# Performance work log

Hardware: AMD Instinct MI355X
Metric: run time of the kernel (lower is better)

The kernel has to match this reference:

```python
import jax, jax.numpy as jnp
import numpy as np

NUM_AUTHORS = 100000
NUM_PAPERS = 150000
EMB_DIM = 64
N_EDGES = 3200000
BATCH = 65536
EPS = 1e-8


def setup_inputs() -> dict:
    key = jax.random.key(0)
    k = jax.random.split(key, 6)
    return {
        "author_emb": jax.random.normal(k[0], (NUM_AUTHORS, EMB_DIM), dtype=jnp.float32) * 0.01,
        "paper_emb": jax.random.normal(k[1], (NUM_PAPERS, EMB_DIM), dtype=jnp.float32) * 0.01,
        "authors": jax.random.randint(k[2], (BATCH,), 0, NUM_AUTHORS),
        "papers": jax.random.randint(k[3], (BATCH,), 0, NUM_PAPERS),
        "edge_author": jax.random.randint(k[4], (N_EDGES,), 0, NUM_AUTHORS),
        "edge_paper": jax.random.randint(k[5], (N_EDGES,), 0, NUM_PAPERS),
    }


def _write_conv(a_emb, p_emb, edge_author, edge_paper, norm, u_sw, i_sw):
    """GCN-style bipartite conv with symmetric degree normalization and
    degree-gated self term (u_sw/i_sw ~= 1 only for isolated nodes)."""
    # messages author -> paper over 'like' edges
    msg_ap = a_emb[edge_author] * norm[:, None]            # [E, D]
    new_p = i_sw * p_emb + jax.ops.segment_sum(msg_ap, edge_paper, num_segments=NUM_PAPERS)
    # messages paper -> author over 'rev_like' edges
    msg_pa = p_emb[edge_paper] * norm[:, None]             # [E, D]
    new_a = u_sw * a_emb + jax.ops.segment_sum(msg_pa, edge_author, num_segments=NUM_AUTHORS)
    return new_a, new_p


def reference(author_emb, paper_emb, authors, papers, edge_author, edge_paper):
    ones_e = jnp.ones((N_EDGES,), dtype=jnp.float32)
    author_deg = jax.ops.segment_sum(ones_e, edge_author, num_segments=NUM_AUTHORS)  # out-deg 'like'
    paper_deg = jax.ops.segment_sum(ones_e, edge_paper, num_segments=NUM_PAPERS)     # out-deg 'rev_like'
    u_sw = (1.0 - author_deg / (author_deg + EPS))[:, None]   # [Na, 1]
    i_sw = (1.0 - paper_deg / (paper_deg + EPS))[:, None]     # [Np, 1]
    # symmetric normalization per edge: 1/sqrt(deg_a * deg_p)
    norm = jax.lax.rsqrt((author_deg[edge_author] + EPS) * (paper_deg[edge_paper] + EPS))  # [E]

    a1, p1 = _write_conv(author_emb, paper_emb, edge_author, edge_paper, norm, u_sw, i_sw)
    a2, p2 = _write_conv(a1, p1, edge_author, edge_paper, norm, u_sw, i_sw)

    final_author = author_emb + a1 + a2   # l_author = [0,1,2]
    final_paper = paper_emb + p1 + p2     # l_paper = [0,1,2]

    latest_author = final_author[authors]  # [B, D]
    latest_paper = final_paper[papers]     # [B, D]
    predict = jax.nn.sigmoid(jnp.sum(latest_author * latest_paper, axis=1))  # [B]
    return predict, latest_author, latest_paper
```

## Files before the change

kernel.cpp:

```cpp
#include <hip/hip_runtime.h>
#include <hip/hip_bf16.h>
#include <math.h>

#define NA 100000
#define NP 150000
#define EMB 64
#define NE 3200000
#define BATCH 65536
#define EPS 1e-8f
#define F8 128.0f
#define INVF8 (1.0f / 128.0f)

#define SH_A 8
#define SH_P 9
#define NB_A ((NA + (1 << SH_A) - 1) >> SH_A)
#define NB_P ((NP + (1 << SH_P) - 1) >> SH_P)
#define NBT (NB_A + NB_P)
#define CAP_A 9216
#define CAP_P 12288
#define TOT_A (NB_A * CAP_A)
#define TOT_P (NB_P * CAP_P)
#define PACK_SH 18
#define PACK_MASK ((1u << PACK_SH) - 1)
#define CHUNK 8192

typedef float f32x2 __attribute__((ext_vector_type(2)));

#if defined(__has_builtin)
#if __has_builtin(__builtin_amdgcn_cvt_pk_f32_fp8) && __has_builtin(__builtin_amdgcn_cvt_pk_fp8_f32)
#define HW_FP8 1
#endif
#endif

__device__ inline unsigned pk_fp8x4(float a, float b, float c, float d) {
#ifdef HW_FP8
    int t = __builtin_amdgcn_cvt_pk_fp8_f32(a, b, 0, false);
    t = __builtin_amdgcn_cvt_pk_fp8_f32(c, d, t, true);
    return (unsigned)t;
#else
    auto enc = [](float x) -> unsigned {
        union { float f; unsigned u; } t; t.f = x;
        unsigned s = t.u >> 31; int e = (int)((t.u >> 23) & 0xFF) - 127;
        unsigned m = (t.u >> 20) & 7;
        int E = e + 7;
        if (E <= 0) return s << 7;
        if (E > 15) { E = 15; m = 7; }
        return (s << 7) | ((unsigned)E << 3) | m;
    };
    return enc(a) | (enc(b) << 8) | (enc(c) << 16) | (enc(d) << 24);
#endif
}

__device__ inline f32x2 up_fp8x2(unsigned v, bool hi) {
#ifdef HW_FP8
    return hi ? __builtin_amdgcn_cvt_pk_f32_fp8((int)v, true)
              : __builtin_amdgcn_cvt_pk_f32_fp8((int)v, false);
#else
    auto dec = [](unsigned b) -> float {
        unsigned s = b >> 7, e = (b >> 3) & 0xF, m = b & 7;
        if (e == 0) return (s ? -1.0f : 1.0f) * (float)m * 0.001953125f;
        union { unsigned u; float f; } t;
        t.u = (s << 31) | ((e + 120) << 23) | (m << 20);
        return t.f;
    };
    unsigned sh = hi ? 16 : 0;
    f32x2 r;
    r.x = dec((v >> sh) & 0xFF);
    r.y = dec((v >> (sh + 8)) & 0xFF);
    return r;
#endif
}

__device__ inline unsigned pack_bf16(float a, float b) {
    __hip_bfloat16 ha = __float2bfloat16(a);
    __hip_bfloat16 hb = __float2bfloat16(b);
    unsigned ua = *(unsigned short*)&ha;
    unsigned ub = *(unsigned short*)&hb;
    return ua | (ub << 16);
}

__device__ inline float bf_lo(unsigned u) { return __uint_as_float(u << 16); }
__device__ inline float bf_hi(unsigned u) { return __uint_as_float(u & 0xffff0000u); }


__global__ void init_cur(int* __restrict__ bcur, uint2* __restrict__ sa0,
                         uint2* __restrict__ sp0, uint2* __restrict__ sa1,
                         uint2* __restrict__ sp1) {
    int i = blockIdx.x * blockDim.x + threadIdx.x;
    if (i < NB_A) bcur[i] = i * CAP_A;
    else if (i < NBT) bcur[i] = (i - NB_A) * CAP_P;
    if (i < 8)       sa0[(size_t)NA * 8 + i]        = uint2{0, 0};
    else if (i < 16) sp0[(size_t)NP * 8 + (i - 8)]  = uint2{0, 0};
    else if (i < 24) sa1[(size_t)NA * 8 + (i - 16)] = uint2{0, 0};
    else if (i < 32) sp1[(size_t)NP * 8 + (i - 24)] = uint2{0, 0};
}


__global__ void stage_kernel(const int* __restrict__ ea, const int* __restrict__ ep,
                             int* __restrict__ bcur,
                             unsigned* __restrict__ stg_a, unsigned* __restrict__ stg_p) {
    __shared__ int h[NBT];
    __shared__ int lcur[NBT];
    int t = threadIdx.x;
    for (int i = t; i < NBT; i += blockDim.x) h[i] = 0;
    __syncthreads();
    int e0 = blockIdx.x * CHUNK;
    int e1 = min(e0 + CHUNK, NE);
    for (int e = e0 + t; e < e1; e += blockDim.x) {
        atomicAdd(&h[ea[e] >> SH_A], 1);
        atomicAdd(&h[NB_A + (ep[e] >> SH_P)], 1);
    }
    __syncthreads();
    for (int i = t; i < NBT; i += blockDim.x) {
        int c = h[i];
        h[i] = c ? atomicAdd(&bcur[i], c) : 0;
        lcur[i] = 0;
    }
    __syncthreads();
    for (int e = e0 + t; e < e1; e += blockDim.x) {
        int a = ea[e], p = ep[e];
        int ba = a >> SH_A;
        int bp = NB_A + (p >> SH_P);
        int la = atomicAdd(&lcur[ba], 1);
        stg_a[h[ba] + la] = ((unsigned)(a & ((1 << SH_A) - 1)) << PACK_SH) | (unsigned)p;
        int lp = atomicAdd(&lcur[bp], 1);
        stg_p[h[bp] + lp] = ((unsigned)(p & ((1 << SH_P) - 1)) << PACK_SH) | (unsigned)a;
    }
}


template <int S, int CAP, int NNODES>
__device__ __forceinline__ void build_side(
    const unsigned* __restrict__ stg, const int* __restrict__ bend, int b,
    int* __restrict__ off, float* __restrict__ rs, int* __restrict__ dg,
    int* __restrict__ csr, const float4* __restrict__ emb, uint2* __restrict__ sfp8,
    int* cnt , int* tsum , int* ls ) {
    constexpr int PER = S / 256;
    int t = threadIdx.x;
    int node0 = b * S;
    int nloc = min(S, NNODES - node0);
    int p0 = b * CAP, p1 = bend[b];
    int nent = p1 - p0;

    for (int i = t; i < S; i += 256) cnt[i] = 0;
    __syncthreads();
    for (int i = p0 + t; i < p1; i += 256)
        atomicAdd(&cnt[stg[i] >> PACK_SH], 1);
    __syncthreads();

    int base_t = t * PER;
    int vals[PER];
    int sum = 0;
    #pragma unroll
    for (int k = 0; k < PER; ++k) { vals[k] = cnt[base_t + k]; sum += vals[k]; }
    tsum[t] = sum;
    __syncthreads();
    for (int o = 1; o < 256; o <<= 1) {
        int v = (t >= o) ? tsum[t - o] : 0;
        __syncthreads();
        tsum[t] += v;
        __syncthreads();
    }
    int excl = (t == 0) ? 0 : tsum[t - 1];
    #pragma unroll
    for (int k = 0; k < PER; ++k) {
        int li = base_t + k;
        if (li < nloc) {
            off[node0 + li] = p0 + excl;
            dg[node0 + li] = vals[k];
            rs[node0 + li] = rsqrtf((float)vals[k] + EPS);
        }
        cnt[li] = excl;
        excl += vals[k];
    }
    __syncthreads();

    for (int i = p0 + t; i < p1; i += 256) {
        unsigned v = stg[i];
        int slot = atomicAdd(&cnt[v >> PACK_SH], 1);
        ls[slot] = (int)((v & PACK_MASK) << 6);
    }
    __syncthreads();

    int rounded = (nent + 3) & ~3;
    for (int i = t * 4; i < rounded; i += 1024) {
        int4 w = {ls[i], ls[i + 1], ls[i + 2], ls[i + 3]};
        *(int4*)(csr + p0 + i) = w;
    }

    int q = t & 7;
    for (int ln = t >> 3; ln < nloc; ln += 32) {
        int n = node0 + ln;
        float r = rs[n] * F8;
        float4 v0 = emb[n * 16 + q * 2];
        float4 v1 = emb[n * 16 + q * 2 + 1];
        uint2 o;
        o.x = pk_fp8x4(r * v0.x, r * v0.y, r * v0.z, r * v0.w);
        o.y = pk_fp8x4(r * v1.x, r * v1.y, r * v1.z, r * v1.w);
        sfp8[(size_t)n * 8 + q] = o;
    }
}

__global__ void build_all(const unsigned* __restrict__ stg_a,
                          const unsigned* __restrict__ stg_p,
                          const int* __restrict__ bcur,
                          int* __restrict__ off_a, float* __restrict__ rs_a,
                          int* __restrict__ dg_a, int* __restrict__ csr_a,
                          int* __restrict__ off_p, float* __restrict__ rs_p,
                          int* __restrict__ dg_p, int* __restrict__ csr_p,
                          const float4* __restrict__ a_emb, const float4* __restrict__ p_emb,
                          uint2* __restrict__ sa0, uint2* __restrict__ sp0) {
    __shared__ int ls[CAP_P];
    __shared__ int cnt[512];
    __shared__ int tsum[256];
    int b = blockIdx.x;
    if (b < NB_A)
        build_side<256, CAP_A, NA>(stg_a, bcur, b, off_a, rs_a, dg_a, csr_a,
                                   a_emb, sa0, cnt, tsum, ls);
    else
        build_side<512, CAP_P, NP>(stg_p, bcur + NB_A, b - NB_A, off_p, rs_p, dg_p, csr_p,
                                   p_emb, sp0, cnt, tsum, ls);
}

template <int LAYER, bool IS_PAPER>
__global__ void pullg(const int* __restrict__ off_s, const int* __restrict__ dg_s,
                      const int* __restrict__ csr_s, const float* __restrict__ rs_s,
                      const uint2* __restrict__ src,
                      const float4* __restrict__ emb,
                      uint4* __restrict__ io,
                      uint2* __restrict__ sout) {
    constexpr int NW = (IS_PAPER ? NP : NA) / 8;
    int wid = (int)(((size_t)blockIdx.x * blockDim.x + threadIdx.x) >> 6);
    if (wid >= NW) return;
    int lane = threadIdx.x & 63;
    int g = lane >> 3;
    int q = lane & 7;
    int n = wid * 8 + g;

    const char* srcb = (const char*)src;
    unsigned zoff = (unsigned)(IS_PAPER ? NA : NP) << 6;

    int start = off_s[n];
    int deg = dg_s[n];
    float rsd = rs_s[n];
    unsigned q8 = (unsigned)(q << 3);

    f32x2 acc[4];
    acc[0] = f32x2{0, 0}; acc[1] = f32x2{0, 0};
    acc[2] = f32x2{0, 0}; acc[3] = f32x2{0, 0};

    unsigned myid_next = (q < deg) ? (unsigned)csr_s[start + q] : zoff;
    for (int t = 0; t < deg; t += 8) {
        unsigned myid = myid_next;
        {
            unsigned idv = (unsigned)csr_s[start + t + 8 + q];
            myid_next = (t + 8 + q < deg) ? idv : zoff;
        }
        uint2 v[8];
        #pragma unroll
        for (int k = 0; k < 8; ++k) {
            unsigned ide = (unsigned)__shfl((int)myid, k, 8);
            v[k] = *(const uint2*)(srcb + (ide | q8));
        }
        #pragma unroll
        for (int k = 0; k < 8; ++k) {
            acc[0] += up_fp8x2(v[k].x, false);
            acc[1] += up_fp8x2(v[k].x, true);
            acc[2] += up_fp8x2(v[k].y, false);
            acc[3] += up_fp8x2(v[k].y, true);
        }
    }

    float inv = rsd * INVF8;
    if (LAYER == 1) {
        int f4 = n * 16 + q * 2;
        float4 e0 = emb[f4];
        float4 e1 = emb[f4 + 1];
        float d = (float)deg;
        float sw = 1.0f - d / (d + EPS);
        float l1[8];
        l1[0] = sw * e0.x + inv * acc[0].x;
        l1[1] = sw * e0.y + inv * acc[0].y;
        l1[2] = sw * e0.z + inv * acc[1].x;
        l1[3] = sw * e0.w + inv * acc[1].y;
        l1[4] = sw * e1.x + inv * acc[2].x;
        l1[5] = sw * e1.y + inv * acc[2].y;
        l1[6] = sw * e1.z + inv * acc[3].x;
        l1[7] = sw * e1.w + inv * acc[3].y;
        float gs = F8 * rsd;
        uint2 sv;
        sv.x = pk_fp8x4(gs * l1[0], gs * l1[1], gs * l1[2], gs * l1[3]);
        sv.y = pk_fp8x4(gs * l1[4], gs * l1[5], gs * l1[6], gs * l1[7]);
        sout[(size_t)n * 8 + q] = sv;
        float c = 1.0f + sw;
        uint4 ov;
        ov.x = pack_bf16(e0.x + c * l1[0], e0.y + c * l1[1]);
        ov.y = pack_bf16(e0.z + c * l1[2], e0.w + c * l1[3]);
        ov.z = pack_bf16(e1.x + c * l1[4], e1.y + c * l1[5]);
        ov.w = pack_bf16(e1.z + c * l1[6], e1.w + c * l1[7]);
        io[(size_t)n * 8 + q] = ov;
    } else {
        uint4 pr = io[(size_t)n * 8 + q];
        uint4 ov;
        ov.x = pack_bf16(bf_lo(pr.x) + inv * acc[0].x, bf_hi(pr.x) + inv * acc[0].y);
        ov.y = pack_bf16(bf_lo(pr.y) + inv * acc[1].x, bf_hi(pr.y) + inv * acc[1].y);
        ov.z = pack_bf16(bf_lo(pr.z) + inv * acc[2].x, bf_hi(pr.z) + inv * acc[2].y);
        ov.w = pack_bf16(bf_lo(pr.w) + inv * acc[3].x, bf_hi(pr.w) + inv * acc[3].y);
        io[(size_t)n * 8 + q] = ov;
    }
}


__global__ void gather_kernel(const unsigned short* __restrict__ fa,
                              const unsigned short* __restrict__ fp,
                              const int* __restrict__ authors, const int* __restrict__ papers,
                              float* __restrict__ out, int batch) {
    int t = blockIdx.x * blockDim.x + threadIdx.x;
    int b = t >> 6;
    int d = t & 63;
    if (b >= batch) return;
    float la = __uint_as_float((unsigned)fa[authors[b] * EMB + d] << 16);
    float lp = __uint_as_float((unsigned)fp[papers[b] * EMB + d] << 16);
    out[batch + b * EMB + d] = la;
    out[batch + batch * EMB + b * EMB + d] = lp;
    float prod = la * lp;
    #pragma unroll
    for (int off = 32; off > 0; off >>= 1)
        prod += __shfl_down(prod, off, 64);
    if (d == 0)
        out[b] = 1.0f / (1.0f + expf(-prod));
}


extern "C" void kernel_launch(void* const* d_in, const int* in_sizes, int n_in,
                              void* d_out, int out_size, void* d_ws, size_t ws_size,
                              hipStream_t stream) {
    const float* author_emb = (const float*)d_in[0];
    const float* paper_emb  = (const float*)d_in[1];
    const int*   authors    = (const int*)d_in[2];
    const int*   papers     = (const int*)d_in[3];
    const int*   edge_a     = (const int*)d_in[4];
    const int*   edge_p     = (const int*)d_in[5];
    float* out = (float*)d_out;

    char* ws = (char*)d_ws;
    size_t woff = 0;
    auto alloc = [&](size_t bytes) {
        void* p = ws + woff;
        woff += (bytes + 255) & ~(size_t)255;
        return p;
    };
    int*   bcur    = (int*)alloc(NBT * sizeof(int));
    int*   off_a   = (int*)alloc(NA * sizeof(int));
    int*   off_p   = (int*)alloc(NP * sizeof(int));
    int*   dg_a    = (int*)alloc(NA * sizeof(int));
    int*   dg_p    = (int*)alloc(NP * sizeof(int));
    float* rs_a    = (float*)alloc(NA * sizeof(float));
    float* rs_p    = (float*)alloc(NP * sizeof(float));
    int*   csr_a   = (int*)alloc((size_t)TOT_A * sizeof(int));
    int*   csr_p   = (int*)alloc((size_t)TOT_P * sizeof(int));
    uint2* sa0     = (uint2*)alloc((size_t)(NA + 1) * EMB);
    uint2* sp0     = (uint2*)alloc((size_t)(NP + 1) * EMB);
    uint2* sa1     = (uint2*)alloc((size_t)(NA + 1) * EMB);
    uint2* sp1     = (uint2*)alloc((size_t)(NP + 1) * EMB);
    uint4* a1      = (uint4*)alloc((size_t)NA * EMB * 2);
    uint4* p1      = (uint4*)alloc((size_t)NP * EMB * 2);
    unsigned* stg_a = (unsigned*)alloc((size_t)TOT_A * sizeof(unsigned));
    unsigned* stg_p = (unsigned*)alloc((size_t)TOT_P * sizeof(unsigned));
    (void)ws_size;

    init_cur<<<(NBT + 255) / 256, 256, 0, stream>>>(bcur, sa0, sp0, sa1, sp1);
    stage_kernel<<<(NE + CHUNK - 1) / CHUNK, 512, 0, stream>>>(edge_a, edge_p, bcur, stg_a, stg_p);
    build_all<<<NBT, 256, 0, stream>>>(stg_a, stg_p, bcur,
                                       off_a, rs_a, dg_a, csr_a,
                                       off_p, rs_p, dg_p, csr_p,
                                       (const float4*)author_emb, (const float4*)paper_emb,
                                       sa0, sp0);

    const unsigned GP = (unsigned)(((long long)(NP / 8) * 64 + 255) / 256);
    const unsigned GA = (unsigned)(((long long)(NA / 8) * 64 + 255) / 256);

    pullg<1, true><<<GP, 256, 0, stream>>>(
        off_p, dg_p, csr_p, rs_p, sa0, (const float4*)paper_emb, p1, sp1);
    pullg<1, false><<<GA, 256, 0, stream>>>(
        off_a, dg_a, csr_a, rs_a, sp0, (const float4*)author_emb, a1, sa1);

    pullg<2, true><<<GP, 256, 0, stream>>>(
        off_p, dg_p, csr_p, rs_p, sa1, (const float4*)paper_emb, p1, nullptr);
    pullg<2, false><<<GA, 256, 0, stream>>>(
        off_a, dg_a, csr_a, rs_a, sp1, (const float4*)author_emb, a1, nullptr);

    {
        long long total = (long long)BATCH * 64;
        gather_kernel<<<(unsigned)((total + 255) / 256), 256, 0, stream>>>(
            (const unsigned short*)a1, (const unsigned short*)p1, authors, papers, out, BATCH);
    }
}
```

Baseline: 307.3 us.

## Stage edge buckets in shared memory and flush with coalesced per-bucket copies

The staging kernel now scatters packed entries into a block-local shared buffer ordered by bucket, using a block-wide prefix scan of the bucket histogram. Each wavefront then copies whole bucket runs to global memory contiguously, replacing the previous per-element random global scatter. This costs a 64KB+ shared buffer per block (lower occupancy), a scan with many barriers, and a fixed 512-thread launch bound.

```diff
diff --git a/kernel.cpp b/kernel.cpp
--- a/kernel.cpp
+++ b/kernel.cpp
@@ -96,35 +96,71 @@
 }
 
 
-__global__ void stage_kernel(const int* __restrict__ ea, const int* __restrict__ ep,
-                             int* __restrict__ bcur,
-                             unsigned* __restrict__ stg_a, unsigned* __restrict__ stg_p) {
-    __shared__ int h[NBT];
-    __shared__ int lcur[NBT];
+__global__ void __launch_bounds__(512) stage_kernel(
+        const int* __restrict__ ea, const int* __restrict__ ep,
+        int* __restrict__ bcur,
+        unsigned* __restrict__ stg_a, unsigned* __restrict__ stg_p) {
+    __shared__ unsigned lsbuf[2 * CHUNK];
+    __shared__ int hh[NBT];
+    __shared__ int lbase[NBT];
+    __shared__ int gbase[NBT];
+    __shared__ int tsum[512];
     int t = threadIdx.x;
-    for (int i = t; i < NBT; i += blockDim.x) h[i] = 0;
+
+    for (int i = t; i < NBT; i += 512) hh[i] = 0;
     __syncthreads();
     int e0 = blockIdx.x * CHUNK;
     int e1 = min(e0 + CHUNK, NE);
-    for (int e = e0 + t; e < e1; e += blockDim.x) {
-        atomicAdd(&h[ea[e] >> SH_A], 1);
-        atomicAdd(&h[NB_A + (ep[e] >> SH_P)], 1);
-    }
-    __syncthreads();
-    for (int i = t; i < NBT; i += blockDim.x) {
-        int c = h[i];
-        h[i] = c ? atomicAdd(&bcur[i], c) : 0;
-        lcur[i] = 0;
-    }
-    __syncthreads();
-    for (int e = e0 + t; e < e1; e += blockDim.x) {
+    for (int e = e0 + t; e < e1; e += 512) {
+        atomicAdd(&hh[ea[e] >> SH_A], 1);
+        atomicAdd(&hh[NB_A + (ep[e] >> SH_P)], 1);
+    }
+    __syncthreads();
+
+    int v0 = (2 * t < NBT) ? hh[2 * t] : 0;
+    int v1 = (2 * t + 1 < NBT) ? hh[2 * t + 1] : 0;
+    tsum[t] = v0 + v1;
+    __syncthreads();
+    for (int o = 1; o < 512; o <<= 1) {
+        int v = (t >= o) ? tsum[t - o] : 0;
+        __syncthreads();
+        tsum[t] += v;
+        __syncthreads();
+    }
+    int excl = (t == 0) ? 0 : tsum[t - 1];
+    if (2 * t < NBT) lbase[2 * t] = excl;
+    if (2 * t + 1 < NBT) lbase[2 * t + 1] = excl + v0;
+    __syncthreads();
+
+    for (int i = t; i < NBT; i += 512) {
+        int c = hh[i];
+        gbase[i] = c ? atomicAdd(&bcur[i], c) : 0;
+    }
+    __syncthreads();
+    for (int i = t; i < NBT; i += 512) hh[i] = lbase[i];
+    __syncthreads();
+
+    for (int e = e0 + t; e < e1; e += 512) {
         int a = ea[e], p = ep[e];
         int ba = a >> SH_A;
         int bp = NB_A + (p >> SH_P);
-        int la = atomicAdd(&lcur[ba], 1);
-        stg_a[h[ba] + la] = ((unsigned)(a & ((1 << SH_A) - 1)) << PACK_SH) | (unsigned)p;
-        int lp = atomicAdd(&lcur[bp], 1);
-        stg_p[h[bp] + lp] = ((unsigned)(p & ((1 << SH_P) - 1)) << PACK_SH) | (unsigned)a;
+        int sa = atomicAdd(&hh[ba], 1);
+        lsbuf[sa] = ((unsigned)(a & ((1 << SH_A) - 1)) << PACK_SH) | (unsigned)p;
+        int sp = atomicAdd(&hh[bp], 1);
+        lsbuf[sp] = ((unsigned)(p & ((1 << SH_P) - 1)) << PACK_SH) | (unsigned)a;
+    }
+    __syncthreads();
+
+    int wv = t >> 6, ln = t & 63;
+    for (int i = wv; i < NBT; i += 8) {
+        int lb = lbase[i];
+        int c = hh[i] - lb;
+        int gb = gbase[i];
+        if (i < NB_A) {
+            for (int j = ln; j < c; j += 64) stg_a[gb + j] = lsbuf[lb + j];
+        } else {
+            for (int j = ln; j < c; j += 64) stg_p[gb + j] = lsbuf[lb + j];
+        }
     }
 }
 
```

Result: faster. 285.0 us (-7.2%).
